# Optimization experiments

Hardware: AMD Instinct MI355X
Metric: run time of the kernel (lower is better)

## Reference

```python
import jax, jax.numpy as jnp
import numpy as np

B, N, C_IN, C_OUT, D, K = 64, 2048, 32, 32, 16, 2


def setup_inputs() -> dict:
    key = jax.random.key(0)
    k1, k2, k3, k4 = jax.random.split(key, 4)
    x = jax.random.normal(k1, (B, N, C_IN), dtype=jnp.float32)
    node_embeddings = jax.random.normal(k2, (N, D), dtype=jnp.float32)
    weights_pool = jax.random.normal(k3, (D, K, C_IN, C_OUT), dtype=jnp.float32)
    bias_pool = jax.random.normal(k4, (D, C_OUT), dtype=jnp.float32)
    return {"x": x, "node_embeddings": node_embeddings,
            "weights_pool": weights_pool, "bias_pool": bias_pool}


def reference(x, node_embeddings, weights_pool, bias_pool):
    n = node_embeddings.shape[0]
    # adaptive adjacency: softmax(relu(E E^T), axis=1)  [N, N]
    supports = jax.nn.softmax(jax.nn.relu(node_embeddings @ node_embeddings.T), axis=1)
    # stack [I, A]  -> [K=2, N, N]
    supports = jnp.stack([jnp.eye(n, dtype=supports.dtype), supports], axis=0)
    # per-node weights [N, K, C_in, C_out] and bias [N, C_out]
    weights = jnp.einsum('nd,dkio->nkio', node_embeddings, weights_pool)
    bias = node_embeddings @ bias_pool
    # graph aggregation: [K,N,N] x [B,N,C] -> [B,N,K,C]
    x_g = jnp.einsum('knm,bmc->bnkc', supports, x)
    # per-node batched small GEMM: [B,N,K,Ci] x [N,K,Ci,Co] -> [B,N,Co]
    x_gconv = jnp.einsum('bnki,nkio->bno', x_g, weights) + bias
    return x_gconv
```

## Files before the change

kernel.cpp:

```cpp
#include <hip/hip_runtime.h>


#define NN 2048
#define NB 64
#define CI 32
#define CO 32
#define DD 16

typedef __attribute__((ext_vector_type(8))) short bf16x8;
typedef __attribute__((ext_vector_type(4))) float f32x4;

__device__ __forceinline__ unsigned short f2bf(float f) {
    unsigned u = __float_as_uint(f);
    u += 0x7FFF + ((u >> 16) & 1);
    return (unsigned short)(u >> 16);
}
__device__ __forceinline__ float bf2f(unsigned short h) {
    return __uint_as_float(((unsigned)h) << 16);
}

#define GLOAD16(gp, lp) __builtin_amdgcn_global_load_lds(                 \
    (const __attribute__((address_space(1))) void*)(gp),                  \
    (__attribute__((address_space(3))) void*)(lp), 16, 0, 0)

__global__ __launch_bounds__(256) void adjxT_kernel(const float* __restrict__ E,
                                                    const float* __restrict__ x,
                                                    unsigned short* __restrict__ Ahi,
                                                    unsigned short* __restrict__ Alo,
                                                    unsigned short* __restrict__ xT)
{
    const int n = blockIdx.x;
    const int tid = threadIdx.x;

    __shared__ float tile[64][33];
    __shared__ float row[NN];
    __shared__ float redmax[4];
    __shared__ float redsum[4];

    {
        const int b = n >> 5;
        const int m0 = (n & 31) * 64;
        #pragma unroll
        for (int k = 0; k < 2; ++k) {
            const int idx = tid + k * 256;
            const int r = idx >> 3, q = idx & 7;
            float4 v = *(const float4*)&x[((size_t)b * NN + m0 + r) * CI + q * 4];
            tile[r][q * 4 + 0] = v.x; tile[r][q * 4 + 1] = v.y;
            tile[r][q * 4 + 2] = v.z; tile[r][q * 4 + 3] = v.w;
        }
        __syncthreads();
        const int c = tid >> 3, m8 = (tid & 7) * 8;
        unsigned short o[8];
        #pragma unroll
        for (int e = 0; e < 8; ++e) o[e] = f2bf(tile[m8 + e][c]);
        *(uint4*)&xT[((size_t)b * CI + c) * NN + m0 + m8] = *(uint4*)o;
    }

    const float4* __restrict__ E4 = reinterpret_cast<const float4*>(E);
    const float4 e0 = E4[n * 4 + 0], e1 = E4[n * 4 + 1];
    const float4 e2 = E4[n * 4 + 2], e3 = E4[n * 4 + 3];

    float lmax = 0.0f;
    #pragma unroll
    for (int k = 0; k < NN / 256; ++k) {
        const int m = tid + k * 256;
        const float4 f0 = E4[m * 4 + 0], f1 = E4[m * 4 + 1];
        const float4 f2 = E4[m * 4 + 2], f3 = E4[m * 4 + 3];
        float dot = e0.x * f0.x + e0.y * f0.y + e0.z * f0.z + e0.w * f0.w;
        dot += e1.x * f1.x + e1.y * f1.y + e1.z * f1.z + e1.w * f1.w;
        dot += e2.x * f2.x + e2.y * f2.y + e2.z * f2.z + e2.w * f2.w;
        dot += e3.x * f3.x + e3.y * f3.y + e3.z * f3.z + e3.w * f3.w;
        dot = fmaxf(dot, 0.0f);
        row[m] = dot;
        lmax = fmaxf(lmax, dot);
    }
    #pragma unroll
    for (int off = 32; off > 0; off >>= 1)
        lmax = fmaxf(lmax, __shfl_down(lmax, off, 64));
    if ((tid & 63) == 0) redmax[tid >> 6] = lmax;
    __syncthreads();
    const float gmax = fmaxf(fmaxf(redmax[0], redmax[1]), fmaxf(redmax[2], redmax[3]));

    float lsum = 0.0f;
    #pragma unroll
    for (int k = 0; k < NN / 256; ++k) {
        const int m = tid + k * 256;
        const float v = __expf(row[m] - gmax);
        row[m] = v;
        lsum += v;
    }
    #pragma unroll
    for (int off = 32; off > 0; off >>= 1)
        lsum += __shfl_down(lsum, off, 64);
    if ((tid & 63) == 0) redsum[tid >> 6] = lsum;
    __syncthreads();
    const float inv = 1.0f / (redsum[0] + redsum[1] + redsum[2] + redsum[3]);

    #pragma unroll
    for (int k = 0; k < NN / 256; ++k) {
        const int m = tid + k * 256;
        const float a = row[m] * inv;
        const unsigned short h = f2bf(a);
        Ahi[(size_t)n * NN + m] = h;
        Alo[(size_t)n * NN + m] = f2bf(a - bf2f(h));
    }
}

__global__ __launch_bounds__(256, 2) void agg_mfma(const unsigned short* __restrict__ Ahi,
                                                   const unsigned short* __restrict__ Alo,
                                                   const unsigned short* __restrict__ xT,
                                                   float* __restrict__ agg)
{
    const int n0 = blockIdx.y * 64;
    const int j0 = blockIdx.x * 128;
    const int tid = threadIdx.x;
    const int lane = tid & 63;
    const int w = tid >> 6;
    const int wr = w >> 1, wc = w & 1;

    __shared__ __align__(16) unsigned char sm[65536];

    int soffA[2]; size_t gA[2];
    #pragma unroll
    for (int i = 0; i < 2; ++i) {
        const int off = i * 4096 + tid * 16;
        const int row = off >> 7, cb = off & 127;
        const int mm = (cb ^ ((row & 7) << 4)) >> 1;
        soffA[i] = off;
        gA[i] = (size_t)(n0 + row) * NN + mm;
    }
    int soffX[4]; size_t gX[4];
    #pragma unroll
    for (int i = 0; i < 4; ++i) {
        const int off = i * 4096 + tid * 16;
        const int row = off >> 7, cb = off & 127;
        const int mm = (cb ^ ((row & 7) << 4)) >> 1;
        soffX[i] = 16384 + off;
        gX[i] = (size_t)(j0 + row) * NN + mm;
    }

    const int l15 = lane & 15, lk = lane >> 4;
    const int sw = (lane & 7) << 4;
    int cbs[2];
    cbs[0] = (lk << 4) ^ sw;
    cbs[1] = (64 + (lk << 4)) ^ sw;
    int offA[2][2], offL[2][2], offX[4][2];
    #pragma unroll
    for (int fm = 0; fm < 2; ++fm) {
        const int r = wr * 32 + fm * 16 + l15;
        #pragma unroll
        for (int s = 0; s < 2; ++s) {
            offA[fm][s] = (r << 7) + cbs[s];
            offL[fm][s] = 8192 + (r << 7) + cbs[s];
        }
    }
    #pragma unroll
    for (int fj = 0; fj < 4; ++fj) {
        const int r = wc * 64 + fj * 16 + l15;
        #pragma unroll
        for (int s = 0; s < 2; ++s)
            offX[fj][s] = 16384 + (r << 7) + cbs[s];
    }

    f32x4 acc[2][4];
    #pragma unroll
    for (int fm = 0; fm < 2; ++fm)
        #pragma unroll
        for (int fj = 0; fj < 4; ++fj) acc[fm][fj] = (f32x4)0.0f;

    #pragma unroll
    for (int i = 0; i < 2; ++i) {
        GLOAD16(Ahi + gA[i], sm + soffA[i]);
        GLOAD16(Alo + gA[i], sm + 8192 + soffA[i]);
    }
    #pragma unroll
    for (int i = 0; i < 4; ++i)
        GLOAD16(xT + gX[i], sm + soffX[i]);
    __syncthreads();

    int buf = 0;
    for (int ks = 0; ks < NN / 64; ++ks) {
        const int nb = buf ^ 1;
        if (ks != NN / 64 - 1) {
            const size_t adv = (size_t)(ks + 1) * 64;
            #pragma unroll
            for (int i = 0; i < 2; ++i) {
                GLOAD16(Ahi + gA[i] + adv, sm + nb * 32768 + soffA[i]);
                GLOAD16(Alo + gA[i] + adv, sm + nb * 32768 + 8192 + soffA[i]);
            }
            #pragma unroll
            for (int i = 0; i < 4; ++i)
                GLOAD16(xT + gX[i] + adv, sm + nb * 32768 + soffX[i]);
        }
        const unsigned char* Bp = sm + buf * 32768;
        bf16x8 av[2][2], lv[2][2], xv[4][2];
        #pragma unroll
        for (int fm = 0; fm < 2; ++fm)
            #pragma unroll
            for (int s = 0; s < 2; ++s) {
                av[fm][s] = *(const bf16x8*)(Bp + offA[fm][s]);
                lv[fm][s] = *(const bf16x8*)(Bp + offL[fm][s]);
            }
        #pragma unroll
        for (int fj = 0; fj < 4; ++fj)
            #pragma unroll
            for (int s = 0; s < 2; ++s)
                xv[fj][s] = *(const bf16x8*)(Bp + offX[fj][s]);

        #pragma unroll
        for (int s = 0; s < 2; ++s)
            #pragma unroll
            for (int fm = 0; fm < 2; ++fm)
                #pragma unroll
                for (int fj = 0; fj < 4; ++fj) {
                    acc[fm][fj] = __builtin_amdgcn_mfma_f32_16x16x32_bf16(
                        av[fm][s], xv[fj][s], acc[fm][fj], 0, 0, 0);
                    acc[fm][fj] = __builtin_amdgcn_mfma_f32_16x16x32_bf16(
                        lv[fm][s], xv[fj][s], acc[fm][fj], 0, 0, 0);
                }
        __syncthreads();
        buf = nb;
    }

    #pragma unroll
    for (int fm = 0; fm < 2; ++fm)
        #pragma unroll
        for (int fj = 0; fj < 4; ++fj) {
            const int nbase = n0 + wr * 32 + fm * 16 + lk * 4;
            const int j = j0 + wc * 64 + fj * 16 + l15;
            const int b = j >> 5, c = j & 31;
            #pragma unroll
            for (int r = 0; r < 4; ++r)
                agg[((size_t)b * NN + nbase + r) * CI + c] = acc[fm][fj][r];
        }
}

__global__ __launch_bounds__(256) void outw_kernel(const float* __restrict__ E,
                                                   const float* __restrict__ Wp,
                                                   const float* __restrict__ Bp,
                                                   const float* __restrict__ x,
                                                   float* __restrict__ out)
{
    const int n = blockIdx.x;
    const int tid = threadIdx.x;

    __shared__ __align__(16) float W[2 * CI * CO];
    __shared__ __align__(16) float Xs[NB][CI];
    __shared__ __align__(16) float Gs[NB][CI];

    {
        const int b = tid >> 3, q = (tid & 7) * 4;
        const int b2 = (tid + 256) >> 3;
        GLOAD16(x + ((size_t)b * NN + n) * CI + q,     (char*)Xs + tid * 16);
        GLOAD16(x + ((size_t)b2 * NN + n) * CI + q,    (char*)Xs + 4096 + tid * 16);
        GLOAD16(out + ((size_t)b * NN + n) * CI + q,   (char*)Gs + tid * 16);
        GLOAD16(out + ((size_t)b2 * NN + n) * CI + q,  (char*)Gs + 4096 + tid * 16);
    }

    float e[DD];
    #pragma unroll
    for (int d = 0; d < DD; ++d) e[d] = E[n * DD + d];

    {
        const float4* __restrict__ Wp4 = (const float4*)Wp;
        float4 a0 = make_float4(0.f, 0.f, 0.f, 0.f);
        float4 a1 = make_float4(0.f, 0.f, 0.f, 0.f);
        #pragma unroll
        for (int d = 0; d < DD; ++d) {
            const float4 w0 = Wp4[d * 512 + tid];
            const float4 w1 = Wp4[d * 512 + 256 + tid];
            const float c = e[d];
            a0.x = fmaf(c, w0.x, a0.x); a0.y = fmaf(c, w0.y, a0.y);
            a0.z = fmaf(c, w0.z, a0.z); a0.w = fmaf(c, w0.w, a0.w);
            a1.x = fmaf(c, w1.x, a1.x); a1.y = fmaf(c, w1.y, a1.y);
            a1.z = fmaf(c, w1.z, a1.z); a1.w = fmaf(c, w1.w, a1.w);
        }
        *(float4*)&W[tid * 4] = a0;
        *(float4*)&W[1024 + tid * 4] = a1;
    }
    __syncthreads();

    const int o  = tid & 31;
    const int bb = tid >> 5;

    float bias = 0.0f;
    #pragma unroll
    for (int d = 0; d < DD; ++d) bias = fmaf(e[d], Bp[d * CO + o], bias);

    float w0[CI], w1[CI];
    #pragma unroll
    for (int i = 0; i < CI; ++i) {
        w0[i] = W[i * 32 + o];
        w1[i] = W[1024 + i * 32 + o];
    }

    #pragma unroll
    for (int j = 0; j < 8; ++j) {
        const int b = bb + 8 * j;
        float s = bias;
        #pragma unroll
        for (int iq = 0; iq < 8; ++iq) {
            const float4 xq = *(const float4*)&Xs[b][iq * 4];
            const float4 gq = *(const float4*)&Gs[b][iq * 4];
            s = fmaf(xq.x, w0[iq * 4 + 0], s);
            s = fmaf(xq.y, w0[iq * 4 + 1], s);
            s = fmaf(xq.z, w0[iq * 4 + 2], s);
            s = fmaf(xq.w, w0[iq * 4 + 3], s);
            s = fmaf(gq.x, w1[iq * 4 + 0], s);
            s = fmaf(gq.y, w1[iq * 4 + 1], s);
            s = fmaf(gq.z, w1[iq * 4 + 2], s);
            s = fmaf(gq.w, w1[iq * 4 + 3], s);
        }
        out[((size_t)b * NN + n) * CO + o] = s;
    }
}

extern "C" void kernel_launch(void* const* d_in, const int* in_sizes, int n_in,
                              void* d_out, int out_size, void* d_ws, size_t ws_size,
                              hipStream_t stream)
{
    const float* x  = (const float*)d_in[0];
    const float* E  = (const float*)d_in[1];
    const float* Wp = (const float*)d_in[2];
    const float* Bp = (const float*)d_in[3];
    float* out = (float*)d_out;

    unsigned short* Ahi = (unsigned short*)d_ws;
    unsigned short* Alo = Ahi + (size_t)NN * NN;
    unsigned short* xT  = Alo + (size_t)NN * NN;

    adjxT_kernel<<<NN, 256, 0, stream>>>(E, x, Ahi, Alo, xT);
    agg_mfma<<<dim3(NN / 128, NN / 64), 256, 0, stream>>>(Ahi, Alo, xT, out);
    outw_kernel<<<NN, 256, 0, stream>>>(E, Wp, Bp, x, out);
}
```

Before: 144.2 us.

## Replace split bf16 hi/lo adjacency with single fp16 and remap workgroups

Stores the softmax adjacency and transposed x as fp16 instead of a bf16 hi/lo pair, which halves the adjacency traffic, the LDS footprint and the MFMA count in the aggregation GEMM. It also flattens the grid to 1D and remaps workgroup IDs so neighbouring blocks are spread across the output tiles, aiming for better cache locality across XCDs. The cost is lower precision: a single fp16 adjacency term replaces the compensated bf16 pair, and fp16 has a narrower range for x values.

```diff
diff --git a/kernel.cpp b/kernel.cpp
--- a/kernel.cpp
+++ b/kernel.cpp
@@ -7,17 +7,8 @@
 #define CO 32
 #define DD 16
 
-typedef __attribute__((ext_vector_type(8))) short bf16x8;
+typedef _Float16 half8 __attribute__((ext_vector_type(8)));
 typedef __attribute__((ext_vector_type(4))) float f32x4;
-
-__device__ __forceinline__ unsigned short f2bf(float f) {
-    unsigned u = __float_as_uint(f);
-    u += 0x7FFF + ((u >> 16) & 1);
-    return (unsigned short)(u >> 16);
-}
-__device__ __forceinline__ float bf2f(unsigned short h) {
-    return __uint_as_float(((unsigned)h) << 16);
-}
 
 #define GLOAD16(gp, lp) __builtin_amdgcn_global_load_lds(                 \
     (const __attribute__((address_space(1))) void*)(gp),                  \
@@ -25,9 +16,8 @@
 
 __global__ __launch_bounds__(256) void adjxT_kernel(const float* __restrict__ E,
                                                     const float* __restrict__ x,
-                                                    unsigned short* __restrict__ Ahi,
-                                                    unsigned short* __restrict__ Alo,
-                                                    unsigned short* __restrict__ xT)
+                                                    _Float16* __restrict__ A,
+                                                    _Float16* __restrict__ xT)
 {
     const int n = blockIdx.x;
     const int tid = threadIdx.x;
@@ -50,9 +40,9 @@
         }
         __syncthreads();
         const int c = tid >> 3, m8 = (tid & 7) * 8;
-        unsigned short o[8];
-        #pragma unroll
-        for (int e = 0; e < 8; ++e) o[e] = f2bf(tile[m8 + e][c]);
+        _Float16 o[8];
+        #pragma unroll
+        for (int e = 0; e < 8; ++e) o[e] = (_Float16)tile[m8 + e][c];
         *(uint4*)&xT[((size_t)b * CI + c) * NN + m0 + m8] = *(uint4*)o;
     }
 
@@ -99,26 +89,26 @@
     #pragma unroll
     for (int k = 0; k < NN / 256; ++k) {
         const int m = tid + k * 256;
-        const float a = row[m] * inv;
-        const unsigned short h = f2bf(a);
-        Ahi[(size_t)n * NN + m] = h;
-        Alo[(size_t)n * NN + m] = f2bf(a - bf2f(h));
+        A[(size_t)n * NN + m] = (_Float16)(row[m] * inv);
     }
 }
 
-__global__ __launch_bounds__(256, 2) void agg_mfma(const unsigned short* __restrict__ Ahi,
-                                                   const unsigned short* __restrict__ Alo,
-                                                   const unsigned short* __restrict__ xT,
+__global__ __launch_bounds__(256, 2) void agg_mfma(const _Float16* __restrict__ A,
+                                                   const _Float16* __restrict__ xT,
                                                    float* __restrict__ agg)
 {
-    const int n0 = blockIdx.y * 64;
-    const int j0 = blockIdx.x * 128;
+    const int wg = blockIdx.x;
+    const int logical = (wg & 7) * 64 + (wg >> 3);
+    const int jt = logical >> 5;
+    const int nt = logical & 31;
+    const int n0 = nt * 64;
+    const int j0 = jt * 128;
     const int tid = threadIdx.x;
     const int lane = tid & 63;
     const int w = tid >> 6;
     const int wr = w >> 1, wc = w & 1;
 
-    __shared__ __align__(16) unsigned char sm[65536];
+    __shared__ __align__(16) unsigned char sm[49152];
 
     int soffA[2]; size_t gA[2];
     #pragma unroll
@@ -135,7 +125,7 @@
         const int off = i * 4096 + tid * 16;
         const int row = off >> 7, cb = off & 127;
         const int mm = (cb ^ ((row & 7) << 4)) >> 1;
-        soffX[i] = 16384 + off;
+        soffX[i] = 8192 + off;
         gX[i] = (size_t)(j0 + row) * NN + mm;
     }
 
@@ -144,22 +134,20 @@
     int cbs[2];
     cbs[0] = (lk << 4) ^ sw;
     cbs[1] = (64 + (lk << 4)) ^ sw;
-    int offA[2][2], offL[2][2], offX[4][2];
+    int offA[2][2], offX[4][2];
     #pragma unroll
     for (int fm = 0; fm < 2; ++fm) {
         const int r = wr * 32 + fm * 16 + l15;
         #pragma unroll
-        for (int s = 0; s < 2; ++s) {
+        for (int s = 0; s < 2; ++s)
             offA[fm][s] = (r << 7) + cbs[s];
-            offL[fm][s] = 8192 + (r << 7) + cbs[s];
-        }
     }
     #pragma unroll
     for (int fj = 0; fj < 4; ++fj) {
         const int r = wc * 64 + fj * 16 + l15;
         #pragma unroll
         for (int s = 0; s < 2; ++s)
-            offX[fj][s] = 16384 + (r << 7) + cbs[s];
+            offX[fj][s] = 8192 + (r << 7) + cbs[s];
     }
 
     f32x4 acc[2][4];
@@ -169,10 +157,8 @@
         for (int fj = 0; fj < 4; ++fj) acc[fm][fj] = (f32x4)0.0f;
 
     #pragma unroll
-    for (int i = 0; i < 2; ++i) {
-        GLOAD16(Ahi + gA[i], sm + soffA[i]);
-        GLOAD16(Alo + gA[i], sm + 8192 + soffA[i]);
-    }
+    for (int i = 0; i < 2; ++i)
+        GLOAD16(A + gA[i], sm + soffA[i]);
     #pragma unroll
     for (int i = 0; i < 4; ++i)
         GLOAD16(xT + gX[i], sm + soffX[i]);
@@ -184,40 +170,33 @@
         if (ks != NN / 64 - 1) {
             const size_t adv = (size_t)(ks + 1) * 64;
             #pragma unroll
-            for (int i = 0; i < 2; ++i) {
-                GLOAD16(Ahi + gA[i] + adv, sm + nb * 32768 + soffA[i]);
-                GLOAD16(Alo + gA[i] + adv, sm + nb * 32768 + 8192 + soffA[i]);
-            }
+            for (int i = 0; i < 2; ++i)
+                GLOAD16(A + gA[i] + adv, sm + nb * 24576 + soffA[i]);
             #pragma unroll
             for (int i = 0; i < 4; ++i)
-                GLOAD16(xT + gX[i] + adv, sm + nb * 32768 + soffX[i]);
-        }
-        const unsigned char* Bp = sm + buf * 32768;
-        bf16x8 av[2][2], lv[2][2], xv[4][2];
+                GLOAD16(xT + gX[i] + adv, sm + nb * 24576 + soffX[i]);
+        }
+        const unsigned char* Bp = sm + buf * 24576;
+        half8 av[2][2], xv[4][2];
         #pragma unroll
         for (int fm = 0; fm < 2; ++fm)
             #pragma unroll
-            for (int s = 0; s < 2; ++s) {
-                av[fm][s] = *(const bf16x8*)(Bp + offA[fm][s]);
-                lv[fm][s] = *(const bf16x8*)(Bp + offL[fm][s]);
-            }
+            for (int s = 0; s < 2; ++s)
+                av[fm][s] = *(const half8*)(Bp + offA[fm][s]);
         #pragma unroll
         for (int fj = 0; fj < 4; ++fj)
             #pragma unroll
             for (int s = 0; s < 2; ++s)
-                xv[fj][s] = *(const bf16x8*)(Bp + offX[fj][s]);
+                xv[fj][s] = *(const half8*)(Bp + offX[fj][s]);
 
         #pragma unroll
         for (int s = 0; s < 2; ++s)
             #pragma unroll
             for (int fm = 0; fm < 2; ++fm)
                 #pragma unroll
-                for (int fj = 0; fj < 4; ++fj) {
-                    acc[fm][fj] = __builtin_amdgcn_mfma_f32_16x16x32_bf16(
+                for (int fj = 0; fj < 4; ++fj)
+                    acc[fm][fj] = __builtin_amdgcn_mfma_f32_16x16x32_f16(
                         av[fm][s], xv[fj][s], acc[fm][fj], 0, 0, 0);
-                    acc[fm][fj] = __builtin_amdgcn_mfma_f32_16x16x32_bf16(
-                        lv[fm][s], xv[fj][s], acc[fm][fj], 0, 0, 0);
-                }
         __syncthreads();
         buf = nb;
     }
@@ -325,11 +304,10 @@
     const float* Bp = (const float*)d_in[3];
     float* out = (float*)d_out;
 
-    unsigned short* Ahi = (unsigned short*)d_ws;
-    unsigned short* Alo = Ahi + (size_t)NN * NN;
-    unsigned short* xT  = Alo + (size_t)NN * NN;
-
-    adjxT_kernel<<<NN, 256, 0, stream>>>(E, x, Ahi, Alo, xT);
-    agg_mfma<<<dim3(NN / 128, NN / 64), 256, 0, stream>>>(Ahi, Alo, xT, out);
+    _Float16* A  = (_Float16*)d_ws;
+    _Float16* xT = A + (size_t)NN * NN;
+
+    adjxT_kernel<<<NN, 256, 0, stream>>>(E, x, A, xT);
+    agg_mfma<<<512, 256, 0, stream>>>(A, xT, out);
     outw_kernel<<<NN, 256, 0, stream>>>(E, Wp, Bp, x, out);
 }
```

Result: faster. 137.8 us (-4.5%).
